# Optimization experiments

Hardware: AMD Instinct MI355X
Metric: run time of the kernel (lower is better)

Reference implementation:

```python
import jax, jax.numpy as jnp
import numpy as np

N = 100_000            # total nodes (many graphs packed together)
E = 1_200_000          # total edges (avg degree 12)
NIN = 3                # input node features (MNISTSuperpixels + degree)
NOUT = 64
NPG = 75               # nodes per graph (nmax=75)
G = (N + NPG - 1) // NPG  # 1334 graphs
EPS = 1e-5


def _dense(k, i, o):
    return jax.random.normal(k, (i, o), jnp.float32) / np.sqrt(i)


def setup_inputs() -> dict:
    key = jax.random.key(0)
    ks = jax.random.split(key, 40)
    inp = {}
    inp["x"] = jax.random.normal(ks[0], (N, NIN), jnp.float32)
    inp["edge_index"] = jax.random.randint(ks[1], (2, E), 0, N, dtype=jnp.int32)
    inp["batch"] = jnp.arange(N, dtype=jnp.int32) // NPG  # sorted graph ids
    # layer 1 params (in=NIN)
    inp["Wc1"] = _dense(ks[2], NIN, NOUT); inp["bc1"] = jnp.zeros((NOUT,), jnp.float32)
    inp["W11"] = _dense(ks[3], NIN, NOUT); inp["b11"] = jnp.zeros((NOUT,), jnp.float32)
    inp["W12"] = _dense(ks[4], NIN, NOUT); inp["b12"] = jnp.zeros((NOUT,), jnp.float32)
    inp["W13"] = _dense(ks[5], NIN, NOUT); inp["b13"] = jnp.zeros((NOUT,), jnp.float32)
    # layer 2 params (in=NOUT)
    inp["Wc2"] = _dense(ks[6], NOUT, NOUT); inp["bc2"] = jnp.zeros((NOUT,), jnp.float32)
    inp["W21"] = _dense(ks[7], NOUT, NOUT); inp["b21"] = jnp.zeros((NOUT,), jnp.float32)
    inp["W22"] = _dense(ks[8], NOUT, NOUT); inp["b22"] = jnp.zeros((NOUT,), jnp.float32)
    inp["W23"] = _dense(ks[9], NOUT, NOUT); inp["b23"] = jnp.zeros((NOUT,), jnp.float32)
    # layer 3 params (in=NOUT)
    inp["Wc3"] = _dense(ks[10], NOUT, NOUT); inp["bc3"] = jnp.zeros((NOUT,), jnp.float32)
    inp["W31"] = _dense(ks[11], NOUT, NOUT); inp["b31"] = jnp.zeros((NOUT,), jnp.float32)
    inp["W32"] = _dense(ks[12], NOUT, NOUT); inp["b32"] = jnp.zeros((NOUT,), jnp.float32)
    inp["W33"] = _dense(ks[13], NOUT, NOUT); inp["b33"] = jnp.zeros((NOUT,), jnp.float32)
    # eval-mode BatchNorm1d on pooled features
    inp["bn_gamma"] = jnp.ones((NOUT,), jnp.float32)
    inp["bn_beta"] = jnp.zeros((NOUT,), jnp.float32)
    inp["bn_mean"] = 0.1 * jax.random.normal(ks[14], (NOUT,), jnp.float32)
    inp["bn_var"] = 0.5 + jax.random.uniform(ks[15], (NOUT,), jnp.float32)
    # classifier head
    inp["Wf1"] = _dense(ks[16], NOUT, 32); inp["bf1"] = jnp.zeros((32,), jnp.float32)
    inp["Wf2"] = _dense(ks[17], 32, 10);  inp["bf2"] = jnp.zeros((10,), jnp.float32)
    return inp


def _layer(x, src, dst, Wc, bc, Wa, ba, Wg1, bg1, Wg2, bg2):
    # SpectConv with edge_attr == 1, selfconn=False: h[dst] += x[src]; then h @ Wc + bc
    agg = jax.ops.segment_sum(x[src], dst, num_segments=N)  # [N, d]
    conv = agg @ Wc + bc
    gate = (x @ Wg1 + bg1) * (x @ Wg2 + bg2)
    return jax.nn.relu(x @ Wa + ba + conv + gate)


def reference(x, edge_index, batch,
              Wc1, bc1, W11, b11, W12, b12, W13, b13,
              Wc2, bc2, W21, b21, W22, b22, W23, b23,
              Wc3, bc3, W31, b31, W32, b32, W33, b33,
              bn_gamma, bn_beta, bn_mean, bn_var,
              Wf1, bf1, Wf2, bf2):
    src, dst = edge_index[0], edge_index[1]  # PyG source_to_target flow
    h = _layer(x, src, dst, Wc1, bc1, W11, b11, W12, b12, W13, b13)
    h = _layer(h, src, dst, Wc2, bc2, W21, b21, W22, b22, W23, b23)
    h = _layer(h, src, dst, Wc3, bc3, W31, b31, W32, b32, W33, b33)
    # global mean pool over graphs
    sums = jax.ops.segment_sum(h, batch, num_segments=G)            # [G, 64]
    cnts = jax.ops.segment_sum(jnp.ones((N,), h.dtype), batch, num_segments=G)
    pooled = sums / jnp.maximum(cnts, 1.0)[:, None]
    # BatchNorm1d (eval mode, running stats)
    z = (pooled - bn_mean) * jax.lax.rsqrt(bn_var + EPS) * bn_gamma + bn_beta
    z = jax.nn.relu(z @ Wf1 + bf1)
    return jax.nn.log_softmax(z @ Wf2 + bf2, axis=1)
```

## Files before the change

### kernel.cpp

```cpp
#include <hip/hip_runtime.h>

#define NN 100000
#define EE 1200000
#define NOUTF 64
#define NPG 75
#define GG 1334
#define BN_EPS 1e-5f
#define NBLK 391

__global__ void hist_kernel(const int* __restrict__ ei, int* __restrict__ deg) {
    int e = blockIdx.x * 256 + threadIdx.x;
    if (e >= EE) return;
    atomicAdd(&deg[ei[EE + e]], 1);
}

__global__ void scan_block(const int* __restrict__ deg, int* __restrict__ row,
                           int* __restrict__ bsum) {
    __shared__ int tmp[256];
    int tid = threadIdx.x;
    int i = blockIdx.x * 256 + tid;
    int v = (i < NN) ? deg[i] : 0;
    tmp[tid] = v;
    __syncthreads();
    for (int off = 1; off < 256; off <<= 1) {
        int t = (tid >= off) ? tmp[tid - off] : 0;
        __syncthreads();
        tmp[tid] += t;
        __syncthreads();
    }
    if (i < NN) row[i] = tmp[tid] - v;
    if (tid == 255) bsum[blockIdx.x] = tmp[255];
}

__global__ void scan_bsums(const int* __restrict__ bsum, int* __restrict__ boff) {
    __shared__ int tmp[512];
    int tid = threadIdx.x;
    int v = (tid < NBLK) ? bsum[tid] : 0;
    tmp[tid] = v;
    __syncthreads();
    for (int off = 1; off < 512; off <<= 1) {
        int t = (tid >= off) ? tmp[tid - off] : 0;
        __syncthreads();
        tmp[tid] += t;
        __syncthreads();
    }
    if (tid < NBLK) boff[tid] = tmp[tid] - v;
}

__global__ void add_off(int* __restrict__ row, const int* __restrict__ boff,
                        int* __restrict__ cursor) {
    int i = blockIdx.x * 256 + threadIdx.x;
    if (i < NN) {
        int r = row[i] + boff[blockIdx.x];
        row[i] = r;
        cursor[i] = r;
    }
    if (i == 0) row[NN] = EE;
}

__global__ void fill_kernel(const int* __restrict__ ei, int* __restrict__ cursor,
                            int* __restrict__ csr) {
    int e = blockIdx.x * 256 + threadIdx.x;
    if (e >= EE) return;
    int d = ei[EE + e];
    int p = atomicAdd(&cursor[d], 1);
    csr[p] = ei[e];
}

__global__ void gather3(const int* __restrict__ row, const int* __restrict__ csr,
                        const float* __restrict__ x, float* __restrict__ agg) {
    int n = blockIdx.x * 256 + threadIdx.x;
    if (n >= NN) return;
    int j0 = row[n], j1 = row[n + 1];
    float a0 = 0, a1 = 0, a2 = 0;
    int j = j0;
    for (; j + 4 <= j1; j += 4) {
        int s0 = csr[j], s1 = csr[j + 1], s2 = csr[j + 2], s3 = csr[j + 3];
        a0 += x[s0 * 3 + 0] + x[s1 * 3 + 0] + x[s2 * 3 + 0] + x[s3 * 3 + 0];
        a1 += x[s0 * 3 + 1] + x[s1 * 3 + 1] + x[s2 * 3 + 1] + x[s3 * 3 + 1];
        a2 += x[s0 * 3 + 2] + x[s1 * 3 + 2] + x[s2 * 3 + 2] + x[s3 * 3 + 2];
    }
    for (; j < j1; j++) {
        int s = csr[j];
        a0 += x[s * 3 + 0]; a1 += x[s * 3 + 1]; a2 += x[s * 3 + 2];
    }
    agg[n * 3 + 0] = a0; agg[n * 3 + 1] = a1; agg[n * 3 + 2] = a2;
}

__global__ void layer1(const float* __restrict__ x, const float* __restrict__ agg,
                       const float* __restrict__ Wc, const float* __restrict__ bc,
                       const float* __restrict__ Wa, const float* __restrict__ ba,
                       const float* __restrict__ W1, const float* __restrict__ b1,
                       const float* __restrict__ W2, const float* __restrict__ b2,
                       float* __restrict__ out) {
    int t = blockIdx.x * 256 + threadIdx.x;
    if (t >= NN * NOUTF) return;
    int n = t >> 6, o = t & 63;
    float x0 = x[n * 3 + 0], x1 = x[n * 3 + 1], x2 = x[n * 3 + 2];
    float a0 = agg[n * 3 + 0], a1 = agg[n * 3 + 1], a2 = agg[n * 3 + 2];
    float lin = fmaf(x0, Wa[o], fmaf(x1, Wa[64 + o], fmaf(x2, Wa[128 + o], ba[o])));
    float cv  = fmaf(a0, Wc[o], fmaf(a1, Wc[64 + o], fmaf(a2, Wc[128 + o], bc[o])));
    float g1  = fmaf(x0, W1[o], fmaf(x1, W1[64 + o], fmaf(x2, W1[128 + o], b1[o])));
    float g2  = fmaf(x0, W2[o], fmaf(x1, W2[64 + o], fmaf(x2, W2[128 + o], b2[o])));
    float v = lin + cv + g1 * g2;
    out[t] = v > 0.0f ? v : 0.0f;
}

__global__ __launch_bounds__(256) void aggl23(
        const int* __restrict__ row, const int* __restrict__ csr,
        const float* __restrict__ h,
        const float* __restrict__ Wc, const float* __restrict__ bc,
        const float* __restrict__ Wa, const float* __restrict__ ba,
        const float* __restrict__ W1, const float* __restrict__ b1,
        const float* __restrict__ W2, const float* __restrict__ b2,
        float* __restrict__ out) {
    __shared__ float hl[16][64];
    __shared__ float al[16][64];
    int n0 = blockIdx.x * 16;
    int tid = threadIdx.x;
    int o = tid & 63;
    int q = tid >> 6;

    ((float4*)&hl[0][0])[tid] = ((const float4*)(h + (size_t)n0 * 64))[tid];

#pragma unroll
    for (int k = 0; k < 4; k++) {
        int n = n0 + q * 4 + k;
        int j0 = row[n], j1 = row[n + 1];
        float acc = 0.0f;
        int j = j0;
        for (; j + 4 <= j1; j += 4) {
            int s0 = csr[j], s1 = csr[j + 1], s2 = csr[j + 2], s3 = csr[j + 3];
            float v0 = h[(size_t)s0 * 64 + o];
            float v1 = h[(size_t)s1 * 64 + o];
            float v2 = h[(size_t)s2 * 64 + o];
            float v3 = h[(size_t)s3 * 64 + o];
            acc += (v0 + v1) + (v2 + v3);
        }
        for (; j < j1; j++) acc += h[(size_t)csr[j] * 64 + o];
        al[q * 4 + k][o] = acc;
    }
    __syncthreads();

    float acc_a[4], acc_c[4], acc_1[4], acc_2[4];
#pragma unroll
    for (int k = 0; k < 4; k++) { acc_a[k] = 0; acc_c[k] = 0; acc_1[k] = 0; acc_2[k] = 0; }
#pragma unroll
    for (int i = 0; i < 64; i += 4) {
        float wa[4], wc[4], w1[4], w2[4];
#pragma unroll
        for (int r = 0; r < 4; r++) {
            wa[r] = Wa[(i + r) * 64 + o];
            wc[r] = Wc[(i + r) * 64 + o];
            w1[r] = W1[(i + r) * 64 + o];
            w2[r] = W2[(i + r) * 64 + o];
        }
#pragma unroll
        for (int k = 0; k < 4; k++) {
            int m = q * 4 + k;
            float4 hv = *(const float4*)&hl[m][i];
            float4 av = *(const float4*)&al[m][i];
            acc_a[k] = fmaf(hv.w, wa[3], fmaf(hv.z, wa[2], fmaf(hv.y, wa[1], fmaf(hv.x, wa[0], acc_a[k]))));
            acc_c[k] = fmaf(av.w, wc[3], fmaf(av.z, wc[2], fmaf(av.y, wc[1], fmaf(av.x, wc[0], acc_c[k]))));
            acc_1[k] = fmaf(hv.w, w1[3], fmaf(hv.z, w1[2], fmaf(hv.y, w1[1], fmaf(hv.x, w1[0], acc_1[k]))));
            acc_2[k] = fmaf(hv.w, w2[3], fmaf(hv.z, w2[2], fmaf(hv.y, w2[1], fmaf(hv.x, w2[0], acc_2[k]))));
        }
    }
    float bao = ba[o], bco = bc[o], b1o = b1[o], b2o = b2[o];
#pragma unroll
    for (int k = 0; k < 4; k++) {
        int m = q * 4 + k;
        float v = acc_a[k] + bao + acc_c[k] + bco + (acc_1[k] + b1o) * (acc_2[k] + b2o);
        out[(size_t)(n0 + m) * 64 + o] = v > 0.0f ? v : 0.0f;
    }
}

__global__ __launch_bounds__(256) void pool_head(
        const float* __restrict__ h,
        const float* __restrict__ gamma, const float* __restrict__ beta,
        const float* __restrict__ mean, const float* __restrict__ var,
        const float* __restrict__ Wf1, const float* __restrict__ bf1,
        const float* __restrict__ Wf2, const float* __restrict__ bf2,
        float* __restrict__ out) {
    __shared__ float part[4][64];
    __shared__ float z[64];
    __shared__ float hid[32];
    __shared__ float logit[10];
    int g = blockIdx.x;
    int tid = threadIdx.x;
    int o = tid & 63, w = tid >> 6;
    int n0 = g * NPG;
    int cnt = NN - n0; if (cnt > NPG) cnt = NPG;
    float s = 0.0f;
    for (int k = w; k < cnt; k += 4) s += h[(size_t)(n0 + k) * 64 + o];
    part[w][o] = s;
    __syncthreads();
    if (tid < 64) {
        float t = (part[0][o] + part[1][o]) + (part[2][o] + part[3][o]);
        t /= (float)cnt;
        z[o] = (t - mean[o]) * rsqrtf(var[o] + BN_EPS) * gamma[o] + beta[o];
    }
    __syncthreads();
    if (tid < 32) {
        float a = bf1[tid];
#pragma unroll
        for (int i = 0; i < 64; i++) a = fmaf(z[i], Wf1[i * 32 + tid], a);
        hid[tid] = a > 0.0f ? a : 0.0f;
    }
    __syncthreads();
    if (tid < 10) {
        float a = bf2[tid];
#pragma unroll
        for (int j = 0; j < 32; j++) a = fmaf(hid[j], Wf2[j * 10 + tid], a);
        logit[tid] = a;
    }
    __syncthreads();
    if (tid < 10) {
        float m = logit[0];
        for (int c = 1; c < 10; c++) m = fmaxf(m, logit[c]);
        float se = 0.0f;
        for (int c = 0; c < 10; c++) se += expf(logit[c] - m);
        out[g * 10 + tid] = logit[tid] - m - logf(se);
    }
}

extern "C" void kernel_launch(void* const* d_in, const int* in_sizes, int n_in,
                              void* d_out, int out_size, void* d_ws, size_t ws_size,
                              hipStream_t stream) {
    const float* x  = (const float*)d_in[0];
    const int*  ei  = (const int*)d_in[1];
    const float *Wc1 = (const float*)d_in[3],  *bc1 = (const float*)d_in[4];
    const float *W11 = (const float*)d_in[5],  *b11 = (const float*)d_in[6];
    const float *W12 = (const float*)d_in[7],  *b12 = (const float*)d_in[8];
    const float *W13 = (const float*)d_in[9],  *b13 = (const float*)d_in[10];
    const float *Wc2 = (const float*)d_in[11], *bc2 = (const float*)d_in[12];
    const float *W21 = (const float*)d_in[13], *b21 = (const float*)d_in[14];
    const float *W22 = (const float*)d_in[15], *b22 = (const float*)d_in[16];
    const float *W23 = (const float*)d_in[17], *b23 = (const float*)d_in[18];
    const float *Wc3 = (const float*)d_in[19], *bc3 = (const float*)d_in[20];
    const float *W31 = (const float*)d_in[21], *b31 = (const float*)d_in[22];
    const float *W32 = (const float*)d_in[23], *b32 = (const float*)d_in[24];
    const float *W33 = (const float*)d_in[25], *b33 = (const float*)d_in[26];
    const float *bng = (const float*)d_in[27], *bnb = (const float*)d_in[28];
    const float *bnm = (const float*)d_in[29], *bnv = (const float*)d_in[30];
    const float *Wf1 = (const float*)d_in[31], *bf1 = (const float*)d_in[32];
    const float *Wf2 = (const float*)d_in[33], *bf2 = (const float*)d_in[34];
    float* out = (float*)d_out;

    float* hA  = (float*)d_ws;
    float* hB  = hA + (size_t)NN * 64;
    int* row    = (int*)(hB + (size_t)NN * 64);
    int* cursor = row + (NN + 2);
    int* bsum   = cursor + NN;
    int* boff   = bsum + 512;
    int* csr    = boff + 512;

    int* deg = cursor;

    hipMemsetAsync(deg, 0, (size_t)NN * sizeof(int), stream);
    hist_kernel<<<(EE + 255) / 256, 256, 0, stream>>>(ei, deg);
    scan_block<<<NBLK, 256, 0, stream>>>(deg, row, bsum);
    scan_bsums<<<1, 512, 0, stream>>>(bsum, boff);
    add_off<<<NBLK, 256, 0, stream>>>(row, boff, cursor);
    fill_kernel<<<(EE + 255) / 256, 256, 0, stream>>>(ei, cursor, csr);

    gather3<<<NBLK, 256, 0, stream>>>(row, csr, x, hB);
    layer1<<<(NN * NOUTF) / 256, 256, 0, stream>>>(x, hB, Wc1, bc1, W11, b11,
                                                   W12, b12, W13, b13, hA);
    aggl23<<<NN / 16, 256, 0, stream>>>(row, csr, hA, Wc2, bc2, W21, b21,
                                        W22, b22, W23, b23, hB);
    aggl23<<<NN / 16, 256, 0, stream>>>(row, csr, hB, Wc3, bc3, W31, b31,
                                        W32, b32, W33, b33, hA);
    pool_head<<<GG, 256, 0, stream>>>(hA, bng, bnb, bnm, bnv, Wf1, bf1, Wf2, bf2, out);
}
```

Before: 584.3 us.

## Gather neighbors with float4 lanes and double nodes per block in layers 2-3

The aggregation phase now splits each wave into four groups of 16 lanes. Each group loads a whole neighbor row as float4s, so four edges are gathered at once, and the partial sums are then combined with cross-lane shuffles. Each block also handles 32 nodes instead of 16, so every weight load is reused across twice as many rows in the dense stage. The aim is to raise memory-level parallelism in the irregular gather and to halve the weight traffic per node. In exchange there are more registers per thread, more shared memory and fewer blocks, which may lower occupancy.

```diff
diff --git a/kernel.cpp b/kernel.cpp
--- a/kernel.cpp
+++ b/kernel.cpp
@@ -114,38 +114,57 @@
         const float* __restrict__ W1, const float* __restrict__ b1,
         const float* __restrict__ W2, const float* __restrict__ b2,
         float* __restrict__ out) {
-    __shared__ float hl[16][64];
-    __shared__ float al[16][64];
-    int n0 = blockIdx.x * 16;
-    int tid = threadIdx.x;
-    int o = tid & 63;
+    __shared__ float hl[32][64];
+    __shared__ float al[32][64];
+    int n0 = blockIdx.x * 32;
+    int tid = threadIdx.x;
     int q = tid >> 6;
-
-    ((float4*)&hl[0][0])[tid] = ((const float4*)(h + (size_t)n0 * 64))[tid];
-
-#pragma unroll
-    for (int k = 0; k < 4; k++) {
-        int n = n0 + q * 4 + k;
+    int l = tid & 63;
+    int g = l >> 4;
+    int c4 = (l & 15) * 4;
+
+    {
+        const float4* hs = (const float4*)(h + (size_t)n0 * 64);
+        float4* hld = (float4*)&hl[0][0];
+#pragma unroll
+        for (int r = 0; r < 8; r++) hld[tid + 256 * r] = hs[tid + 256 * r];
+    }
+
+#pragma unroll 1
+    for (int k = 0; k < 8; k++) {
+        int n = n0 + q * 8 + k;
         int j0 = row[n], j1 = row[n + 1];
-        float acc = 0.0f;
+        float4 acc = make_float4(0.f, 0.f, 0.f, 0.f);
         int j = j0;
-        for (; j + 4 <= j1; j += 4) {
-            int s0 = csr[j], s1 = csr[j + 1], s2 = csr[j + 2], s3 = csr[j + 3];
-            float v0 = h[(size_t)s0 * 64 + o];
-            float v1 = h[(size_t)s1 * 64 + o];
-            float v2 = h[(size_t)s2 * 64 + o];
-            float v3 = h[(size_t)s3 * 64 + o];
-            acc += (v0 + v1) + (v2 + v3);
-        }
-        for (; j < j1; j++) acc += h[(size_t)csr[j] * 64 + o];
-        al[q * 4 + k][o] = acc;
-    }
-    __syncthreads();
-
-    float acc_a[4], acc_c[4], acc_1[4], acc_2[4];
-#pragma unroll
-    for (int k = 0; k < 4; k++) { acc_a[k] = 0; acc_c[k] = 0; acc_1[k] = 0; acc_2[k] = 0; }
-#pragma unroll
+        for (; j + 8 <= j1; j += 8) {
+            int sA = csr[j + g];
+            int sB = csr[j + 4 + g];
+            float4 vA = *(const float4*)(h + (size_t)sA * 64 + c4);
+            float4 vB = *(const float4*)(h + (size_t)sB * 64 + c4);
+            acc.x += vA.x + vB.x; acc.y += vA.y + vB.y;
+            acc.z += vA.z + vB.z; acc.w += vA.w + vB.w;
+        }
+        for (; j < j1; j += 4) {
+            int jj = j + g;
+            if (jj < j1) {
+                int s = csr[jj];
+                float4 v = *(const float4*)(h + (size_t)s * 64 + c4);
+                acc.x += v.x; acc.y += v.y; acc.z += v.z; acc.w += v.w;
+            }
+        }
+        acc.x += __shfl_xor(acc.x, 16); acc.y += __shfl_xor(acc.y, 16);
+        acc.z += __shfl_xor(acc.z, 16); acc.w += __shfl_xor(acc.w, 16);
+        acc.x += __shfl_xor(acc.x, 32); acc.y += __shfl_xor(acc.y, 32);
+        acc.z += __shfl_xor(acc.z, 32); acc.w += __shfl_xor(acc.w, 32);
+        if (g == 0) *(float4*)&al[q * 8 + k][c4] = acc;
+    }
+    __syncthreads();
+
+    int o = l;
+    float acc_a[8], acc_c[8], acc_1[8], acc_2[8];
+#pragma unroll
+    for (int k = 0; k < 8; k++) { acc_a[k] = 0; acc_c[k] = 0; acc_1[k] = 0; acc_2[k] = 0; }
+#pragma unroll 4
     for (int i = 0; i < 64; i += 4) {
         float wa[4], wc[4], w1[4], w2[4];
 #pragma unroll
@@ -156,8 +175,8 @@
             w2[r] = W2[(i + r) * 64 + o];
         }
 #pragma unroll
-        for (int k = 0; k < 4; k++) {
-            int m = q * 4 + k;
+        for (int k = 0; k < 8; k++) {
+            int m = q * 8 + k;
             float4 hv = *(const float4*)&hl[m][i];
             float4 av = *(const float4*)&al[m][i];
             acc_a[k] = fmaf(hv.w, wa[3], fmaf(hv.z, wa[2], fmaf(hv.y, wa[1], fmaf(hv.x, wa[0], acc_a[k]))));
@@ -168,8 +187,8 @@
     }
     float bao = ba[o], bco = bc[o], b1o = b1[o], b2o = b2[o];
 #pragma unroll
-    for (int k = 0; k < 4; k++) {
-        int m = q * 4 + k;
+    for (int k = 0; k < 8; k++) {
+        int m = q * 8 + k;
         float v = acc_a[k] + bao + acc_c[k] + bco + (acc_1[k] + b1o) * (acc_2[k] + b2o);
         out[(size_t)(n0 + m) * 64 + o] = v > 0.0f ? v : 0.0f;
     }
@@ -267,9 +286,9 @@
     gather3<<<NBLK, 256, 0, stream>>>(row, csr, x, hB);
     layer1<<<(NN * NOUTF) / 256, 256, 0, stream>>>(x, hB, Wc1, bc1, W11, b11,
                                                    W12, b12, W13, b13, hA);
-    aggl23<<<NN / 16, 256, 0, stream>>>(row, csr, hA, Wc2, bc2, W21, b21,
+    aggl23<<<NN / 32, 256, 0, stream>>>(row, csr, hA, Wc2, bc2, W21, b21,
                                         W22, b22, W23, b23, hB);
-    aggl23<<<NN / 16, 256, 0, stream>>>(row, csr, hB, Wc3, bc3, W31, b31,
+    aggl23<<<NN / 32, 256, 0, stream>>>(row, csr, hB, Wc3, bc3, W31, b31,
                                         W32, b32, W33, b33, hA);
     pool_head<<<GG, 256, 0, stream>>>(hA, bng, bnb, bnm, bnv, Wf1, bf1, Wf2, bf2, out);
 }
```

Result: faster. 559.9 us (-4.2%).
